# Kernel tuning notes

Measured on AMD Instinct MI355X. Metric: run time of the kernel, lower is better.

## Reference

```python
import jax, jax.numpy as jnp
import numpy as np

D = 768      # embed_dim
P = 16       # patch size
NP = 14      # patches per side
L = 197      # seq len (196 patches + CLS)
H = 12       # heads
HD = D // H  # head dim
DEPTH = 12
B = 32
ALPHA = 0.5
EPS = 1e-5


def layer_norm(x, g, b):
    m = x.mean(-1, keepdims=True)
    v = ((x - m) ** 2).mean(-1, keepdims=True)
    return g * (x - m) / jnp.sqrt(v + EPS) + b


def patch_embed(x, w, b, g, beta):
    # x: [B, C, 224, 224]; w: [D, C, P, P] (Conv2d stride=P == patchify + matmul)
    Bx, C = x.shape[0], x.shape[1]
    p = x.reshape(Bx, C, NP, P, NP, P).transpose(0, 2, 4, 1, 3, 5).reshape(Bx, NP * NP, C * P * P)
    t = p @ w.reshape(D, -1).T + b
    return layer_norm(t, g, beta)


def setup_inputs() -> dict:
    key = jax.random.key(0)
    ks = jax.random.split(key, 24)
    rn = lambda k, shape, s=0.02: (jax.random.normal(k, shape, jnp.float32) * s)
    inp = {
        'img': jax.random.normal(ks[0], (B, 3, 224, 224), jnp.float32),
        'mask': jax.random.uniform(ks[1], (B, 224, 224), jnp.float32),
        'pe_img_w': rn(ks[2], (D, 3, P, P)), 'pe_img_b': jnp.zeros((D,), jnp.float32),
        'pe_img_g': jnp.ones((D,), jnp.float32), 'pe_img_bb': jnp.zeros((D,), jnp.float32),
        'pe_msk_w': rn(ks[3], (D, 1, P, P)), 'pe_msk_b': jnp.zeros((D,), jnp.float32),
        'pe_msk_g': jnp.ones((D,), jnp.float32), 'pe_msk_bb': jnp.zeros((D,), jnp.float32),
        'cls': rn(ks[4], (1, 1, D)),
        'pos': rn(ks[5], (1, L, D)),
        'ln1_g': jnp.ones((DEPTH, D), jnp.float32), 'ln1_b': jnp.zeros((DEPTH, D), jnp.float32),
        'w_qkv': rn(ks[6], (DEPTH, 3 * D, D)), 'b_qkv': jnp.zeros((DEPTH, 3 * D), jnp.float32),
        'w_out': rn(ks[7], (DEPTH, D, D)), 'b_out': jnp.zeros((DEPTH, D), jnp.float32),
        'ln2_g': jnp.ones((DEPTH, D), jnp.float32), 'ln2_b': jnp.zeros((DEPTH, D), jnp.float32),
        'w_fc1': rn(ks[8], (DEPTH, 4 * D, D)), 'b_fc1': jnp.zeros((DEPTH, 4 * D), jnp.float32),
        'w_fc2': rn(ks[9], (DEPTH, D, 4 * D)), 'b_fc2': jnp.zeros((DEPTH, D), jnp.float32),
        'enc_g': jnp.ones((D,), jnp.float32), 'enc_b': jnp.zeros((D,), jnp.float32),
        'fin_g': jnp.ones((D,), jnp.float32), 'fin_b': jnp.zeros((D,), jnp.float32),
        'head_w': rn(ks[10], (4, D)), 'head_b': jnp.zeros((4,), jnp.float32),
    }
    return inp


def reference(img, mask, pe_img_w, pe_img_b, pe_img_g, pe_img_bb,
              pe_msk_w, pe_msk_b, pe_msk_g, pe_msk_bb, cls, pos,
              ln1_g, ln1_b, w_qkv, b_qkv, w_out, b_out, ln2_g, ln2_b,
              w_fc1, b_fc1, w_fc2, b_fc2, enc_g, enc_b, fin_g, fin_b,
              head_w, head_b):
    Bx = img.shape[0]
    tok_i = patch_embed(img, pe_img_w, pe_img_b, pe_img_g, pe_img_bb)
    tok_m = patch_embed(mask[:, None], pe_msk_w, pe_msk_b, pe_msk_g, pe_msk_bb)
    tokens = tok_i + ALPHA * tok_m                       # [B, 196, D]
    x = jnp.concatenate([jnp.broadcast_to(cls, (Bx, 1, D)), tokens], axis=1) + pos  # [B, L, D]
    # low-rank outer-product attention bias, zero on CLS row/col
    bias_p = jnp.einsum('bid,bjd->bij', tok_m, tok_m) / jnp.sqrt(jnp.float32(D))
    bias = jnp.pad(bias_p, ((0, 0), (1, 0), (1, 0)))     # [B, L, L]

    def block(x, p):
        l1g, l1b, wqkv, bqkv, wo, bo, l2g, l2b, w1, b1, w2, b2 = p
        h = layer_norm(x, l1g, l1b)
        qkv = h @ wqkv.T + bqkv                          # [B, L, 3D]
        q, k, v = jnp.split(qkv, 3, axis=-1)
        hds = lambda t: t.reshape(Bx, L, H, HD).transpose(0, 2, 1, 3)
        q, k, v = hds(q), hds(k), hds(v)                 # [B, H, L, HD]
        s = jnp.einsum('bhid,bhjd->bhij', q, k) / jnp.sqrt(jnp.float32(HD)) + bias[:, None]
        a = jax.nn.softmax(s, axis=-1)
        o = jnp.einsum('bhij,bhjd->bhid', a, v).transpose(0, 2, 1, 3).reshape(Bx, L, D)
        x = x + o @ wo.T + bo
        h2 = layer_norm(x, l2g, l2b)
        x = x + jax.nn.gelu(h2 @ w1.T + b1, approximate=False) @ w2.T + b2
        return x, None

    x, _ = jax.lax.scan(block, x, (ln1_g, ln1_b, w_qkv, b_qkv, w_out, b_out,
                                   ln2_g, ln2_b, w_fc1, b_fc1, w_fc2, b_fc2))
    x = layer_norm(x, enc_g, enc_b)   # ViTEncoder.norm
    x = layer_norm(x, fin_g, fin_b)   # MaskedViT.norm
    return x[:, 0] @ head_w.T + head_b  # [B, num_classes]
```

## Files before the change

### kernel.cpp

```cpp
#include <hip/hip_runtime.h>
#include <hip/hip_bf16.h>
#include <math.h>

typedef unsigned int   u32;
typedef unsigned short u16;
typedef __bf16 bf16x8 __attribute__((ext_vector_type(8)));
typedef float  f32x4  __attribute__((ext_vector_type(4)));
typedef u16    u16x8  __attribute__((ext_vector_type(8)));
typedef u16    u16x4  __attribute__((ext_vector_type(4)));

constexpr int BB = 32, DD = 768, LL = 197, HH = 12, NTOK = 196;
constexpr int MROWS = BB * LL;
constexpr int MTOK  = BB * NTOK;
constexpr long long LLDD = (long long)LL * DD;

__device__ __forceinline__ u16 f2bf(float f) {
    union { float f; u32 u; } v; v.f = f;
    u32 r = v.u + 0x7fff + ((v.u >> 16) & 1);
    return (u16)(r >> 16);
}
__device__ __forceinline__ float bf2f(u16 u) {
    union { u32 u; float f; } v; v.u = ((u32)u) << 16;
    return v.f;
}

#define AS1 __attribute__((address_space(1)))
#define AS3 __attribute__((address_space(3)))
__device__ __forceinline__ void gload_lds16(const void* g, void* l) {
    __builtin_amdgcn_global_load_lds((const AS1 u32*)g, (AS3 u32*)l, 16, 0, 0);
}

__global__ void cast_kernel(const float* __restrict__ in, u16* __restrict__ out, int n)
{
    int i4 = (blockIdx.x * 256 + threadIdx.x) * 4;
    if (i4 >= n) return;
    float4 v = *reinterpret_cast<const float4*>(in + i4);
    out[i4]   = f2bf(v.x); out[i4+1] = f2bf(v.y);
    out[i4+2] = f2bf(v.z); out[i4+3] = f2bf(v.w);
}

__global__ void cast4_kernel(const float* s0, int n0, const float* s1, int n1,
                             const float* s2, int n2, const float* s3, int n3,
                             u16* d0, u16* d1, u16* d2, u16* d3)
{
    int i4 = (blockIdx.x * 256 + threadIdx.x) * 4;
    const float* s; u16* d; int off;
    if      (i4 < n0)            { s = s0; d = d0; off = i4; }
    else if (i4 < n0+n1)         { s = s1; d = d1; off = i4 - n0; }
    else if (i4 < n0+n1+n2)      { s = s2; d = d2; off = i4 - n0 - n1; }
    else if (i4 < n0+n1+n2+n3)   { s = s3; d = d3; off = i4 - n0 - n1 - n2; }
    else return;
    float4 v = *reinterpret_cast<const float4*>(s + off);
    d[off]   = f2bf(v.x); d[off+1] = f2bf(v.y);
    d[off+2] = f2bf(v.z); d[off+3] = f2bf(v.w);
}

__global__ void patchify_kernel(const float* __restrict__ src, int C,
                                u16* __restrict__ out, int total)
{
    int idx = blockIdx.x * 256 + threadIdx.x;
    if (idx >= total) return;
    int K = C * 256;
    int row = idx / K, k = idx % K;
    int b = row / NTOK, n = row % NTOK;
    int c = k >> 8, rem = k & 255, pi = rem >> 4, pj = rem & 15;
    int i14 = n / 14, j14 = n % 14;
    float v = src[(((size_t)b * C + c) * 224 + i14 * 16 + pi) * 224 + j14 * 16 + pj];
    out[idx] = f2bf(v);
}

template<int MODE>
__global__ __launch_bounds__(512) void gemm_bf16(
    const u16* __restrict__ A, const u16* __restrict__ W,
    const float* __restrict__ bias, const float* __restrict__ res,
    void* __restrict__ Cout, int M, int N, int K, long long strideA,
    long long rsA, long long rsC)
{
    __shared__ u16 As[2][8192];
    __shared__ u16 Bs[2][4096];
    const int tid  = threadIdx.x;
    const int wave = tid >> 6, lane = tid & 63;
    const int lo = lane & 15, hi = lane >> 4;
    const int wr = wave >> 1, wc = wave & 1;

    const int m0 = blockIdx.y * 256, n0 = blockIdx.x * 128;
    if (MODE == 3) { A += blockIdx.z * strideA; W += blockIdx.z * strideA; }

    const int Klen = (MODE == 5) ? (K >> 1) : K;
    const int kb   = (MODE == 5) ? blockIdx.z * Klen : 0;

    const int limA = M - 1;
    const int limB = (MODE == 3 ? M : N) - 1;
    const int srow = lane >> 2;
    const int scol = ((lane & 3) ^ ((lane >> 3) & 3)) << 3;
    int ra0 = m0 + wave * 16 + srow;        if (ra0 > limA) ra0 = limA;
    int ra1 = m0 + 128 + wave * 16 + srow;  if (ra1 > limA) ra1 = limA;
    int rb0 = n0 + wave * 16 + srow;        if (rb0 > limB) rb0 = limB;
    const u16* Arow0 = A + (size_t)ra0 * rsA + kb + scol;
    const u16* Arow1 = A + (size_t)ra1 * rsA + kb + scol;
    const u16* Brow0 = W + (size_t)rb0 * K + kb + scol;

    const int fro = lo * 32 + ((hi ^ ((lo >> 1) & 3)) << 3);

    f32x4 acc[4][4] = {};

    #define STAGE(bf_, k0_)                                         \
        do {                                                        \
            gload_lds16(Arow0 + (k0_), &As[bf_][wave * 512]);       \
            gload_lds16(Arow1 + (k0_), &As[bf_][4096 + wave * 512]);\
            gload_lds16(Brow0 + (k0_), &Bs[bf_][wave * 512]);       \
        } while (0)

    #define COMPUTE(bf_)                                                         \
        do {                                                                     \
            bf16x8 af[4], bfr[4];                                                \
            _Pragma("unroll")                                                    \
            for (int i = 0; i < 4; ++i)                                          \
                af[i] = *reinterpret_cast<const bf16x8*>(                        \
                    &As[bf_][(wr * 4 + i) * 512 + fro]);                         \
            _Pragma("unroll")                                                    \
            for (int j = 0; j < 4; ++j)                                          \
                bfr[j] = *reinterpret_cast<const bf16x8*>(                       \
                    &Bs[bf_][(wc * 4 + j) * 512 + fro]);                         \
            _Pragma("unroll")                                                    \
            for (int i = 0; i < 4; ++i)                                          \
                _Pragma("unroll")                                                \
                for (int j = 0; j < 4; ++j)                                      \
                    acc[i][j] = __builtin_amdgcn_mfma_f32_16x16x32_bf16(         \
                        af[i], bfr[j], acc[i][j], 0, 0, 0);                      \
        } while (0)

    const int nt = Klen >> 5;
    STAGE(0, 0);
    __syncthreads();
    int t = 0;
    for (; t + 2 < nt; t += 2) {
        STAGE(1, (t + 1) * 32);
        COMPUTE(0);
        __syncthreads();
        STAGE(0, (t + 2) * 32);
        COMPUTE(1);
        __syncthreads();
    }
    STAGE(1, (t + 1) * 32);
    COMPUTE(0);
    __syncthreads();
    COMPUTE(1);
    #undef STAGE
    #undef COMPUTE

    const size_t zoff = (MODE == 5) ? (size_t)blockIdx.z * M * rsC : 0;
    const int cr = hi * 4;
    const int cc = lo;
    #pragma unroll
    for (int i = 0; i < 4; ++i) {
        #pragma unroll
        for (int r = 0; r < 4; ++r) {
            int m = m0 + wr * 64 + i * 16 + cr + r;
            if (MODE != 3 && m >= M) continue;
            #pragma unroll
            for (int j = 0; j < 4; ++j) {
                int n = n0 + wc * 64 + j * 16 + cc;
                float v = acc[i][j][r];
                if (MODE == 0) {
                    ((float*)Cout)[(size_t)m * rsC + n] = v + bias[n];
                } else if (MODE == 1) {
                    float t2 = v + bias[n];
                    t2 = 0.5f * t2 * (1.f + erff(t2 * 0.70710678118654752f));
                    ((u16*)Cout)[(size_t)m * rsC + n] = f2bf(t2);
                } else if (MODE == 2) {
                    ((float*)Cout)[(size_t)m * rsC + n] = v + bias[n] + res[(size_t)m * rsC + n];
                } else if (MODE == 4) {
                    ((u16*)Cout)[(size_t)m * rsC + n] = f2bf(v + bias[n]);
                } else if (MODE == 5) {
                    ((float*)Cout)[zoff + (size_t)m * rsC + n] = v;
                } else {
                    if (m < M && n < M) {
                        float* C3 = (float*)Cout + (size_t)blockIdx.z * LL * LL;
                        C3[(size_t)(m + 1) * LL + (n + 1)] = v * 0.03608439182435161f;
                    }
                }
            }
        }
    }
}

__global__ void splitk_reduce_kernel(float* __restrict__ x, const float* __restrict__ p,
                                     const float* __restrict__ bias, int MN, int N)
{
    int i4 = (blockIdx.x * 256 + threadIdx.x) * 4;
    if (i4 >= MN) return;
    float4 a  = *reinterpret_cast<const float4*>(x + i4);
    float4 p0 = *reinterpret_cast<const float4*>(p + i4);
    float4 p1 = *reinterpret_cast<const float4*>(p + (size_t)MN + i4);
    float4 b  = *reinterpret_cast<const float4*>(bias + (i4 % N));
    a.x += p0.x + p1.x + b.x;
    a.y += p0.y + p1.y + b.y;
    a.z += p0.z + p1.z + b.z;
    a.w += p0.w + p1.w + b.w;
    *reinterpret_cast<float4*>(x + i4) = a;
}

__global__ __launch_bounds__(256) void reduce_ln_kernel(
    float* __restrict__ x, const float* __restrict__ p,
    const float* __restrict__ bias,
    const float* __restrict__ g, const float* __restrict__ beta,
    u16* __restrict__ outb, int nrows)
{
    int row = blockIdx.x * 4 + (threadIdx.x >> 6);
    if (row >= nrows) return;
    int lane = threadIdx.x & 63;
    size_t MN = (size_t)nrows * DD;
    float4 v[3];
    #pragma unroll
    for (int pp = 0; pp < 3; ++pp) {
        int d0 = pp * 256 + lane * 4;
        size_t ix = (size_t)row * DD + d0;
        float4 xv = *reinterpret_cast<const float4*>(x + ix);
        float4 p0 = *reinterpret_cast<const float4*>(p + ix);
        float4 p1 = *reinterpret_cast<const float4*>(p + MN + ix);
        float4 bv = *reinterpret_cast<const float4*>(bias + d0);
        xv.x += p0.x + p1.x + bv.x;
        xv.y += p0.y + p1.y + bv.y;
        xv.z += p0.z + p1.z + bv.z;
        xv.w += p0.w + p1.w + bv.w;
        *reinterpret_cast<float4*>(x + ix) = xv;
        v[pp] = xv;
    }
    float s = 0.f;
    #pragma unroll
    for (int pp = 0; pp < 3; ++pp) s += v[pp].x + v[pp].y + v[pp].z + v[pp].w;
    #pragma unroll
    for (int off = 32; off; off >>= 1) s += __shfl_xor(s, off);
    float mean = s * (1.f / 768.f);
    float q = 0.f;
    #pragma unroll
    for (int pp = 0; pp < 3; ++pp) {
        float a = v[pp].x - mean, b = v[pp].y - mean, c = v[pp].z - mean, d = v[pp].w - mean;
        q += a * a + b * b + c * c + d * d;
    }
    #pragma unroll
    for (int off = 32; off; off >>= 1) q += __shfl_xor(q, off);
    float rstd = rsqrtf(q * (1.f / 768.f) + 1e-5f);
    #pragma unroll
    for (int pp = 0; pp < 3; ++pp) {
        int d0 = pp * 256 + lane * 4;
        float4 gg = *reinterpret_cast<const float4*>(g + d0);
        float4 bb = *reinterpret_cast<const float4*>(beta + d0);
        u16x4 ob = { f2bf(gg.x * (v[pp].x - mean) * rstd + bb.x),
                     f2bf(gg.y * (v[pp].y - mean) * rstd + bb.y),
                     f2bf(gg.z * (v[pp].z - mean) * rstd + bb.z),
                     f2bf(gg.w * (v[pp].w - mean) * rstd + bb.w) };
        *reinterpret_cast<u16x4*>(outb + (size_t)row * DD + d0) = ob;
    }
}

__global__ void bias_edge_kernel(float* __restrict__ bias)
{
    int b = blockIdx.x, t = threadIdx.x;
    if (t < LL) {
        bias[((size_t)b * LL + 0) * LL + t] = 0.f;
        bias[((size_t)b * LL + t) * LL + 0] = 0.f;
    }
}

__global__ void combine_kernel(
    const float* __restrict__ toki, const float* __restrict__ tokm,
    const float* __restrict__ cls, const float* __restrict__ pos,
    float* __restrict__ x)
{
    size_t idx = (size_t)blockIdx.x * 256 + threadIdx.x;
    if (idx >= (size_t)MROWS * DD) return;
    int d = (int)(idx % DD);
    size_t bl = idx / DD;
    int l = (int)(bl % LL);
    int b = (int)(bl / LL);
    float v;
    if (l == 0) v = cls[d];
    else {
        size_t tix = ((size_t)b * NTOK + (l - 1)) * DD + d;
        v = toki[tix] + 0.5f * tokm[tix];
    }
    x[idx] = v + pos[(size_t)l * DD + d];
}

template<int OUT>
__global__ __launch_bounds__(256) void ln_kernel(
    const float* __restrict__ in, const float* __restrict__ g,
    const float* __restrict__ beta, float* __restrict__ outf,
    u16* __restrict__ outb, int nrows, long long inStride)
{
    int row = blockIdx.x * 4 + (threadIdx.x >> 6);
    if (row >= nrows) return;
    int lane = threadIdx.x & 63;
    const float* xr = in + (size_t)row * inStride;
    float4 v[3];
    #pragma unroll
    for (int p = 0; p < 3; ++p)
        v[p] = *reinterpret_cast<const float4*>(xr + p * 256 + lane * 4);
    float s = 0.f;
    #pragma unroll
    for (int p = 0; p < 3; ++p) s += v[p].x + v[p].y + v[p].z + v[p].w;
    #pragma unroll
    for (int off = 32; off; off >>= 1) s += __shfl_xor(s, off);
    float mean = s * (1.f / 768.f);
    float q = 0.f;
    #pragma unroll
    for (int p = 0; p < 3; ++p) {
        float a = v[p].x - mean, b = v[p].y - mean, c = v[p].z - mean, d = v[p].w - mean;
        q += a * a + b * b + c * c + d * d;
    }
    #pragma unroll
    for (int off = 32; off; off >>= 1) q += __shfl_xor(q, off);
    float rstd = rsqrtf(q * (1.f / 768.f) + 1e-5f);
    #pragma unroll
    for (int p = 0; p < 3; ++p) {
        int d0 = p * 256 + lane * 4;
        float4 gg = *reinterpret_cast<const float4*>(g + d0);
        float4 bb = *reinterpret_cast<const float4*>(beta + d0);
        float o0 = gg.x * (v[p].x - mean) * rstd + bb.x;
        float o1 = gg.y * (v[p].y - mean) * rstd + bb.y;
        float o2 = gg.z * (v[p].z - mean) * rstd + bb.z;
        float o3 = gg.w * (v[p].w - mean) * rstd + bb.w;
        if (OUT == 0 || OUT == 2) {
            float4 of = make_float4(o0, o1, o2, o3);
            *reinterpret_cast<float4*>(outf + (size_t)row * DD + d0) = of;
        }
        if (OUT == 1 || OUT == 2) {
            u16x4 ob = { f2bf(o0), f2bf(o1), f2bf(o2), f2bf(o3) };
            *reinterpret_cast<u16x4*>(outb + (size_t)row * DD + d0) = ob;
        }
    }
}

constexpr int KSTRE = 72;
constexpr int VSTRE = 232;
constexpr int PSTRE = 232;

__global__ __launch_bounds__(512) void attn_mfma_kernel(
    const u16* __restrict__ qkv, const float* __restrict__ bias,
    u16* __restrict__ o)
{
    const int h = blockIdx.x, b = blockIdx.y;
    const int tid = threadIdx.x, wave = tid >> 6, lane = tid & 63;
    const int lo = lane & 15, hi = lane >> 4;

    __shared__ u16 Ks[208 * KSTRE];
    __shared__ u16 Vt[64 * VSTRE];
    __shared__ u16 Ps[8][16 * PSTRE];

    const u16* qb = qkv + (size_t)b * LL * 2304;

    for (int idx = tid; idx < 208 * 8; idx += 512) {
        int key = idx >> 3, c8 = idx & 7;
        u16x8 v = {};
        if (key < LL) v = *reinterpret_cast<const u16x8*>(qb + (size_t)key * 2304 + 768 + h * 64 + c8 * 8);
        *reinterpret_cast<u16x8*>(&Ks[key * KSTRE + c8 * 8]) = v;
    }
    for (int idx = tid; idx < 224 * 8; idx += 512) {
        int key = idx >> 3, c8 = idx & 7;
        u16x8 v = {};
        if (key < LL) v = *reinterpret_cast<const u16x8*>(qb + (size_t)key * 2304 + 1536 + h * 64 + c8 * 8);
        #pragma unroll
        for (int e = 0; e < 8; ++e) Vt[(c8 * 8 + e) * VSTRE + key] = v[e];
    }
    __syncthreads();

    u16* P = Ps[wave];
    const float* biasbb = bias + (size_t)b * LL * LL;

    for (int rt = wave; rt < 13; rt += 8) {
        int q = rt * 16 + lo; if (q > LL - 1) q = LL - 1;
        const u16* qrow = qb + (size_t)q * 2304 + h * 64;
        bf16x8 qa0 = *reinterpret_cast<const bf16x8*>(qrow + hi * 8);
        bf16x8 qa1 = *reinterpret_cast<const bf16x8*>(qrow + 32 + hi * 8);

        f32x4 st[13];
        #pragma unroll
        for (int t = 0; t < 13; ++t) {
            int keyc = t * 16 + lo;
            bf16x8 kb0 = *reinterpret_cast<const bf16x8*>(&Ks[keyc * KSTRE + hi * 8]);
            bf16x8 kb1 = *reinterpret_cast<const bf16x8*>(&Ks[keyc * KSTRE + 32 + hi * 8]);
            f32x4 a = {};
            a = __builtin_amdgcn_mfma_f32_16x16x32_bf16(qa0, kb0, a, 0, 0, 0);
            a = __builtin_amdgcn_mfma_f32_16x16x32_bf16(qa1, kb1, a, 0, 0, 0);
            st[t] = a;
        }

        #pragma unroll
        for (int r = 0; r < 4; ++r) {
            int qq = rt * 16 + hi * 4 + r;
            int qc = qq > LL - 1 ? LL - 1 : qq;
            const float* brow = biasbb + (size_t)qc * LL;
            float s[13];
            float m = -1e30f;
            #pragma unroll
            for (int t = 0; t < 13; ++t) {
                int col = t * 16 + lo;
                float v;
                if (col < LL) v = st[t][r] * 0.125f + brow[col];
                else          v = -1e30f;
                s[t] = v;
                m = fmaxf(m, v);
            }
            m = fmaxf(m, __shfl_xor(m, 1));
            m = fmaxf(m, __shfl_xor(m, 2));
            m = fmaxf(m, __shfl_xor(m, 4));
            m = fmaxf(m, __shfl_xor(m, 8));
            float sum = 0.f;
            #pragma unroll
            for (int t = 0; t < 13; ++t) { float e = __expf(s[t] - m); s[t] = e; sum += e; }
            sum += __shfl_xor(sum, 1);
            sum += __shfl_xor(sum, 2);
            sum += __shfl_xor(sum, 4);
            sum += __shfl_xor(sum, 8);
            float inv = 1.f / sum;
            int prow = (hi * 4 + r) * PSTRE;
            #pragma unroll
            for (int t = 0; t < 13; ++t) P[prow + t * 16 + lo] = f2bf(s[t] * inv);
            P[prow + 208 + lo] = 0;
        }

        f32x4 oacc[4] = {};
        #pragma unroll
        for (int kt = 0; kt < 7; ++kt) {
            bf16x8 pa = *reinterpret_cast<const bf16x8*>(&P[lo * PSTRE + kt * 32 + hi * 8]);
            #pragma unroll
            for (int dt = 0; dt < 4; ++dt) {
                bf16x8 vb = *reinterpret_cast<const bf16x8*>(&Vt[(dt * 16 + lo) * VSTRE + kt * 32 + hi * 8]);
                oacc[dt] = __builtin_amdgcn_mfma_f32_16x16x32_bf16(pa, vb, oacc[dt], 0, 0, 0);
            }
        }

        #pragma unroll
        for (int dt = 0; dt < 4; ++dt) {
            #pragma unroll
            for (int r = 0; r < 4; ++r) {
                int qq = rt * 16 + hi * 4 + r;
                if (qq < LL)
                    o[((size_t)(b * LL + qq)) * DD + h * 64 + dt * 16 + lo] = f2bf(oacc[dt][r]);
            }
        }
    }
}

__global__ __launch_bounds__(256) void final_kernel(
    const float* __restrict__ x,
    const float* __restrict__ eg, const float* __restrict__ eb,
    const float* __restrict__ fg, const float* __restrict__ fb,
    const float* __restrict__ hw, const float* __restrict__ hb,
    float* __restrict__ out)
{
    int b = blockIdx.x;
    int tid = threadIdx.x;
    __shared__ float xs[768];
    __shared__ float red[256];
    const float* xr = x + (size_t)b * LL * DD;
    #pragma unroll
    for (int r = 0; r < 3; ++r) xs[tid + r * 256] = xr[tid + r * 256];
    __syncthreads();
    for (int pass = 0; pass < 2; ++pass) {
        const float* g  = pass ? fg : eg;
        const float* bb = pass ? fb : eb;
        red[tid] = xs[tid] + xs[tid + 256] + xs[tid + 512];
        __syncthreads();
        for (int off = 128; off; off >>= 1) {
            if (tid < off) red[tid] += red[tid + off];
            __syncthreads();
        }
        float mean = red[0] * (1.f / 768.f);
        __syncthreads();
        float q = 0.f;
        #pragma unroll
        for (int r = 0; r < 3; ++r) { float dv = xs[tid + r * 256] - mean; q += dv * dv; }
        red[tid] = q;
        __syncthreads();
        for (int off = 128; off; off >>= 1) {
            if (tid < off) red[tid] += red[tid + off];
            __syncthreads();
        }
        float rstd = rsqrtf(red[0] * (1.f / 768.f) + 1e-5f);
        __syncthreads();
        #pragma unroll
        for (int r = 0; r < 3; ++r) {
            int d = tid + r * 256;
            xs[d] = g[d] * (xs[d] - mean) * rstd + bb[d];
        }
        __syncthreads();
    }
    int c = tid >> 6, lane = tid & 63;
    float part = 0.f;
    for (int d = lane; d < 768; d += 64) part += xs[d] * hw[c * 768 + d];
    #pragma unroll
    for (int off = 32; off; off >>= 1) part += __shfl_down(part, off);
    if (lane == 0) out[b * 4 + c] = part + hb[c];
}

extern "C" void kernel_launch(void* const* d_in, const int* in_sizes, int n_in,
                              void* d_out, int out_size, void* d_ws, size_t ws_size,
                              hipStream_t stream)
{
    const float* img    = (const float*)d_in[0];
    const float* mask   = (const float*)d_in[1];
    const float* pe_iw  = (const float*)d_in[2];
    const float* pe_ib  = (const float*)d_in[3];
    const float* pe_ig  = (const float*)d_in[4];
    const float* pe_ibb = (const float*)d_in[5];
    const float* pe_mw  = (const float*)d_in[6];
    const float* pe_mb  = (const float*)d_in[7];
    const float* pe_mg  = (const float*)d_in[8];
    const float* pe_mbb = (const float*)d_in[9];
    const float* cls    = (const float*)d_in[10];
    const float* pos    = (const float*)d_in[11];
    const float* ln1_g  = (const float*)d_in[12];
    const float* ln1_b  = (const float*)d_in[13];
    const float* w_qkv  = (const float*)d_in[14];
    const float* b_qkv  = (const float*)d_in[15];
    const float* w_out  = (const float*)d_in[16];
    const float* b_out  = (const float*)d_in[17];
    const float* ln2_g  = (const float*)d_in[18];
    const float* ln2_b  = (const float*)d_in[19];
    const float* w_fc1  = (const float*)d_in[20];
    const float* b_fc1  = (const float*)d_in[21];
    const float* w_fc2  = (const float*)d_in[22];
    const float* b_fc2  = (const float*)d_in[23];
    const float* enc_g  = (const float*)d_in[24];
    const float* enc_b  = (const float*)d_in[25];
    const float* fin_g  = (const float*)d_in[26];
    const float* fin_b  = (const float*)d_in[27];
    const float* head_w = (const float*)d_in[28];
    const float* head_b = (const float*)d_in[29];

    char* wsb = (char*)d_ws;
    size_t off = 0;
    auto alloc = [&](size_t bytes) { void* p = wsb + off; off += (bytes + 255) & ~(size_t)255; return p; };

    float* x     = (float*)alloc((size_t)MROWS * DD * 4);
    u16*   qkvb  = (u16*)  alloc((size_t)MROWS * 3 * DD * 2);
    u16*   hbuf  = (u16*)  alloc((size_t)MROWS * DD * 2);
    u16*   fc1b  = (u16*)  alloc((size_t)MROWS * 4 * DD * 2);
    float* biasb = (float*)alloc((size_t)BB * LL * LL * 4);
    u16*   wqb   = (u16*)  alloc((size_t)3 * DD * DD * 2);
    u16*   wob   = (u16*)  alloc((size_t)DD * DD * 2);
    u16*   w1b   = (u16*)  alloc((size_t)4 * DD * DD * 2);
    u16*   w2b   = (u16*)  alloc((size_t)4 * DD * DD * 2);
    float* scratch2 = (float*)alloc((size_t)2 * MROWS * DD * 4);
    float* toki  = scratch2;
    float* tokm  = scratch2 + (size_t)MTOK * DD;
    float* partf = scratch2;
    u16*   pa    = fc1b;
    float* ttmp  = (float*)qkvb;
    u16*   tokmb = hbuf;

    cast_kernel<<<(DD * DD / 4 + 255) / 256, 256, 0, stream>>>(pe_iw, wob, DD * DD);
    patchify_kernel<<<(MTOK * DD + 255) / 256, 256, 0, stream>>>(img, 3, pa, MTOK * DD);
    gemm_bf16<0><<<dim3(DD / 128, (MTOK + 255) / 256), 512, 0, stream>>>(
        pa, wob, pe_ib, nullptr, ttmp, MTOK, DD, DD, 0, DD, DD);
    ln_kernel<0><<<MTOK / 4, 256, 0, stream>>>(ttmp, pe_ig, pe_ibb, toki, nullptr, MTOK, DD);

    cast_kernel<<<(DD * 256 / 4 + 255) / 256, 256, 0, stream>>>(pe_mw, wob, DD * 256);
    patchify_kernel<<<(MTOK * 256 + 255) / 256, 256, 0, stream>>>(mask, 1, pa, MTOK * 256);
    gemm_bf16<0><<<dim3(DD / 128, (MTOK + 255) / 256), 512, 0, stream>>>(
        pa, wob, pe_mb, nullptr, ttmp, MTOK, DD, 256, 0, 256, DD);
    ln_kernel<2><<<MTOK / 4, 256, 0, stream>>>(ttmp, pe_mg, pe_mbb, tokm, tokmb, MTOK, DD);

    gemm_bf16<3><<<dim3(2, 1, BB), 512, 0, stream>>>(
        tokmb, tokmb, nullptr, nullptr, biasb, NTOK, NTOK, DD, (long long)NTOK * DD, DD, DD);
    bias_edge_kernel<<<BB, 256, 0, stream>>>(biasb);

    combine_kernel<<<(MROWS * DD + 255) / 256, 256, 0, stream>>>(toki, tokm, cls, pos, x);
    ln_kernel<1><<<MROWS / 4, 256, 0, stream>>>(x, ln1_g, ln1_b, nullptr, hbuf, MROWS, DD);

    const int mblk = (MROWS + 255) / 256;
    const int wqn = 3 * DD * DD, won = DD * DD, w1n = 4 * DD * DD, w2n = 4 * DD * DD;
    const int castTot = (wqn + won + w1n + w2n) / 4;
    for (int l = 0; l < 12; ++l) {
        cast4_kernel<<<(castTot + 255) / 256, 256, 0, stream>>>(
            w_qkv + (size_t)l * wqn, wqn, w_out + (size_t)l * won, won,
            w_fc1 + (size_t)l * w1n, w1n, w_fc2 + (size_t)l * w2n, w2n,
            wqb, wob, w1b, w2b);
        gemm_bf16<4><<<dim3(3 * DD / 128, mblk), 512, 0, stream>>>(
            hbuf, wqb, b_qkv + l * 3 * DD, nullptr, qkvb, MROWS, 3 * DD, DD, 0, DD, 3 * DD);
        attn_mfma_kernel<<<dim3(HH, BB), 512, 0, stream>>>(qkvb, biasb, hbuf);
        if (l < 11) {
            gemm_bf16<5><<<dim3(DD / 128, mblk, 2), 512, 0, stream>>>(
                hbuf, wob, nullptr, nullptr, partf, MROWS, DD, DD, 0, DD, DD);
            reduce_ln_kernel<<<MROWS / 4, 256, 0, stream>>>(
                x, partf, b_out + l * DD, ln2_g + l * DD, ln2_b + l * DD, hbuf, MROWS);
            gemm_bf16<1><<<dim3(4 * DD / 128, mblk), 512, 0, stream>>>(
                hbuf, w1b, b_fc1 + l * 4 * DD, nullptr, fc1b, MROWS, 4 * DD, DD, 0, DD, 4 * DD);
            gemm_bf16<5><<<dim3(DD / 128, mblk, 2), 512, 0, stream>>>(
                fc1b, w2b, nullptr, nullptr, partf, MROWS, DD, 4 * DD, 0, 4 * DD, DD);
            reduce_ln_kernel<<<MROWS / 4, 256, 0, stream>>>(
                x, partf, b_fc2 + l * DD, ln1_g + (l + 1) * DD, ln1_b + (l + 1) * DD,
                hbuf, MROWS);
        } else {
            gemm_bf16<2><<<dim3(DD / 128, 1), 512, 0, stream>>>(
                hbuf, wob, b_out + l * DD, x, x, BB, DD, DD, 0, LLDD, LLDD);
            ln_kernel<1><<<BB / 4, 256, 0, stream>>>(
                x, ln2_g + l * DD, ln2_b + l * DD, nullptr, hbuf, BB, LLDD);
            gemm_bf16<1><<<dim3(4 * DD / 128, 1), 512, 0, stream>>>(
                hbuf, w1b, b_fc1 + l * 4 * DD, nullptr, fc1b, BB, 4 * DD, DD, 0, DD, 4 * DD);
            gemm_bf16<2><<<dim3(DD / 128, 1), 512, 0, stream>>>(
                fc1b, w2b, b_fc2 + l * DD, x, x, BB, DD, 4 * DD, 0, 4 * DD, LLDD);
        }
    }
    final_kernel<<<BB, 256, 0, stream>>>(x, enc_g, enc_b, fin_g, fin_b, head_w, head_b, (float*)d_out);
}
```

Baseline: 3.169 ms.

## Prefetch two K-tiles ahead in GEMM with explicit vmcnt waits and raw barriers

Restructures the bf16 GEMM main loop so that two K-tiles are staged before compute starts, and each iteration refills the buffer it just consumed two steps ahead. Synchronisation now uses explicit `s_waitcnt vmcnt(3)`/`vmcnt(0)` plus raw `s_barrier`, wrapped in scheduling barriers, instead of `__syncthreads`. The goal is to keep global-to-LDS loads in flight across the MFMA compute and avoid full memory drains at each barrier. Correctness depends on STAGE issuing exactly three vector-memory ops per tile, and the scheduling barriers constrain the compiler's own reordering.

```diff
diff --git a/kernel.cpp b/kernel.cpp
--- a/kernel.cpp
+++ b/kernel.cpp
@@ -68,6 +68,14 @@
     float v = src[(((size_t)b * C + c) * 224 + i14 * 16 + pi) * 224 + j14 * 16 + pj];
     out[idx] = f2bf(v);
 }
+
+#define SBAR()  do { __builtin_amdgcn_sched_barrier(0);                    \
+                     asm volatile("s_barrier" ::: "memory");               \
+                     __builtin_amdgcn_sched_barrier(0); } while (0)
+#define WAITV3() do { asm volatile("s_waitcnt vmcnt(3)" ::: "memory");     \
+                      __builtin_amdgcn_sched_barrier(0); } while (0)
+#define WAITV0() do { asm volatile("s_waitcnt vmcnt(0)" ::: "memory");     \
+                      __builtin_amdgcn_sched_barrier(0); } while (0)
 
 template<int MODE>
 __global__ __launch_bounds__(512) void gemm_bf16(
@@ -132,20 +140,20 @@
 
     const int nt = Klen >> 5;
     STAGE(0, 0);
-    __syncthreads();
-    int t = 0;
-    for (; t + 2 < nt; t += 2) {
-        STAGE(1, (t + 1) * 32);
-        COMPUTE(0);
-        __syncthreads();
-        STAGE(0, (t + 2) * 32);
-        COMPUTE(1);
-        __syncthreads();
-    }
-    STAGE(1, (t + 1) * 32);
-    COMPUTE(0);
-    __syncthreads();
-    COMPUTE(1);
+    STAGE(1, 32);
+    WAITV3();
+    SBAR();
+    for (int t = 0; t < nt; ++t) {
+        COMPUTE(t & 1);
+        SBAR();
+        if (t + 2 < nt) {
+            STAGE(t & 1, (t + 2) * 32);
+            WAITV3();
+        } else {
+            WAITV0();
+        }
+        SBAR();
+    }
     #undef STAGE
     #undef COMPUTE
 
```

New measurement: 3.128 ms. About the same (-1.3%).
